# Kernel optimization log

Measured on AMD Instinct MI355X. Metric: run time of the kernel, lower is better.

The kernel has to match this reference:

```python
import jax, jax.numpy as jnp
import numpy as np

B, L = 4096, 4096

# 16 power-series exponents applied to each of the 4 physical params
PS_POWERS = jnp.array([-5.0, -4.0, -3.0, -2.0, -1.5, -1.0, -0.5, 0.0,
                       0.5, 2.0, 1.0/3.0, 3.0, 0.25, 4.0, 0.2, 5.0], dtype=jnp.float32)
# polynomial exponents of the ansatz y(eta)
POLY_POWERS = jnp.array([2.0, 5.0, 8.0, 11.0, 14.0], dtype=jnp.float32)


def setup_inputs() -> dict:
    key = jax.random.key(0)
    k1, k2, k3, k4, k5, k6 = jax.random.split(key, 6)
    # positive inputs: negative/fractional powers require x > 0
    physical_params = jax.random.uniform(k1, (B, 4), jnp.float32, minval=0.1, maxval=2.0)
    eta = jax.random.uniform(k2, (B, L), jnp.float32, minval=0.1, maxval=2.0)
    # MLP params: Linear(64, 32) and Linear(32, 5), torch layout [out, in]
    W1 = jax.random.normal(k3, (32, 64), jnp.float32) * (1.0 / np.sqrt(64.0))
    b1 = jax.random.normal(k4, (32,), jnp.float32) * 0.05
    W2 = jax.random.normal(k5, (5, 32), jnp.float32) * (1.0 / np.sqrt(32.0))
    b2 = jax.random.normal(k6, (5,), jnp.float32) * 0.05
    return {"physical_params": physical_params, "eta": eta,
            "W1": W1, "b1": b1, "W2": W2, "b2": b2}


def reference(physical_params, eta, W1, b1, W2, b2):
    # power-series transform: [B,4] -> [B,4,16] -> [B,64]
    t = (physical_params[:, :, None] ** PS_POWERS).reshape(physical_params.shape[0], -1)
    # global (scalar) normalization; torch .std() is unbiased (ddof=1)
    mean = t.mean()
    std = jnp.std(t, ddof=1)
    norm = (t - mean) / std
    # network = Sequential(ReLU, Linear(64,32), Linear(32,5)) -- ReLU first, no act between linears
    h = jnp.maximum(norm, 0.0) @ W1.T + b1            # [B, 32]
    coefficients = h @ W2.T + b2                       # [B, 5]
    # dy/deta[i,j] = sum_k c[i,k] * p_k * eta[i,j]^(p_k - 1)  (vectorizes the per-row loop)
    eta_pows = eta[:, :, None] ** (POLY_POWERS - 1.0)  # [B, L, 5]
    dy_deta = jnp.einsum('bk,bjk->bj', coefficients * POLY_POWERS, eta_pows)  # [B, L]
    return dy_deta
```

## Files before the change

### kernel.cpp

```cpp
#include <hip/hip_runtime.h>
#include <math.h>

static constexpr int B  = 4096;
static constexpr int L  = 4096;
static constexpr int NX = B * 4;
static constexpr int STATS_THREADS = 1024;

typedef float f4 __attribute__((ext_vector_type(4)));

__device__ __constant__ float c_ps_powers[16] = {
    -5.0f, -4.0f, -3.0f, -2.0f, -1.5f, -1.0f, -0.5f, 0.0f,
     0.5f,  2.0f,  0.33333334f, 3.0f, 0.25f, 4.0f, 0.2f, 5.0f};

__device__ __constant__ float c_poly[5] = {2.0f, 5.0f, 8.0f, 11.0f, 14.0f};

__device__ __forceinline__ float hw_log2(float x) { return __builtin_amdgcn_logf(x); }
__device__ __forceinline__ float hw_exp2(float x) { return __builtin_amdgcn_exp2f(x); }

__global__ __launch_bounds__(STATS_THREADS)
void k_stats(const float* __restrict__ pp, float* __restrict__ stats) {
    const int tid = threadIdx.x;
    const f4* pp4 = reinterpret_cast<const f4*>(pp);
    double s = 0.0, s2 = 0.0;
    #pragma unroll
    for (int k = 0; k < NX / 4 / STATS_THREADS; ++k) {
        const f4 xv = pp4[tid + k * STATS_THREADS];
        #pragma unroll
        for (int c = 0; c < 4; ++c) {
            const float lx = hw_log2(xv[c]);
            float sf = 0.0f, sf2 = 0.0f;
            #pragma unroll
            for (int p = 0; p < 16; ++p) {
                const float t = hw_exp2(c_ps_powers[p] * lx);
                sf  += t;
                sf2 = fmaf(t, t, sf2);
            }
            s  += (double)sf;
            s2 += (double)sf2;
        }
    }
    __shared__ double sh_s[STATS_THREADS];
    __shared__ double sh_s2[STATS_THREADS];
    sh_s[tid] = s; sh_s2[tid] = s2;
    __syncthreads();
    for (int off = STATS_THREADS >> 1; off > 0; off >>= 1) {
        if (tid < off) {
            sh_s[tid]  += sh_s[tid + off];
            sh_s2[tid] += sh_s2[tid + off];
        }
        __syncthreads();
    }
    if (tid == 0) {
        const double n    = (double)(B * 64);
        const double mean = sh_s[0] / n;
        const double var  = (sh_s2[0] - n * mean * mean) / (n - 1.0);
        stats[0] = (float)mean;
        stats[1] = (float)(1.0 / sqrt(var));
    }
}

__device__ __forceinline__ float poly_eval(float e, float c0, float c1,
                                           float c2, float c3, float c4) {
    const float e3 = e * e * e;
    float w   = e;
    float acc = c0 * w;
    w *= e3;
    acc = fmaf(c1, w, acc);
    w *= e3;
    acc = fmaf(c2, w, acc);
    w *= e3;
    acc = fmaf(c3, w, acc);
    w *= e3;
    acc = fmaf(c4, w, acc);
    return acc;
}

__device__ __forceinline__ f4 poly_eval4(f4 e, float c0, float c1,
                                         float c2, float c3, float c4) {
    f4 r;
    r.x = poly_eval(e.x, c0, c1, c2, c3, c4);
    r.y = poly_eval(e.y, c0, c1, c2, c3, c4);
    r.z = poly_eval(e.z, c0, c1, c2, c3, c4);
    r.w = poly_eval(e.w, c0, c1, c2, c3, c4);
    return r;
}

__global__ __launch_bounds__(256)
void k_main(const float* __restrict__ pp,  const float* __restrict__ eta,
            const float* __restrict__ W1,  const float* __restrict__ b1,
            const float* __restrict__ W2,  const float* __restrict__ b2,
            const float* __restrict__ stats, float* __restrict__ out) {
    const int row = blockIdx.x;
    const int tid = threadIdx.x;

    const f4* ep = reinterpret_cast<const f4*>(eta + (size_t)row * L);
    f4*       op = reinterpret_cast<f4*>(out + (size_t)row * L);
    const f4 e0 = ep[tid];
    const f4 e1 = ep[tid + 256];
    const f4 e2 = ep[tid + 512];
    const f4 e3 = ep[tid + 768];

    __shared__ float sh_r[64];
    __shared__ float sh_h[32];
    __shared__ float sh_c[8];

    if (tid < 64) {
        const float mean    = stats[0];
        const float inv_std = stats[1];
        const float x = pp[(row << 2) + (tid >> 4)];
        const float t = hw_exp2(c_ps_powers[tid & 15] * hw_log2(x));
        sh_r[tid] = fmaxf((t - mean) * inv_std, 0.0f);
    }
    __syncthreads();

    if (tid < 32) {
        float acc = b1[tid];
        const float* w = W1 + tid * 64;
        #pragma unroll
        for (int j = 0; j < 64; ++j) acc = fmaf(sh_r[j], w[j], acc);
        sh_h[tid] = acc;
    }
    __syncthreads();

    if (tid < 5) {
        float acc = b2[tid];
        const float* w = W2 + tid * 32;
        #pragma unroll
        for (int o = 0; o < 32; ++o) acc = fmaf(sh_h[o], w[o], acc);
        sh_c[tid] = acc * c_poly[tid];
    }
    __syncthreads();

    const float c0 = sh_c[0], c1 = sh_c[1], c2 = sh_c[2],
                c3 = sh_c[3], c4 = sh_c[4];

    op[tid]       = poly_eval4(e0, c0, c1, c2, c3, c4);
    op[tid + 256] = poly_eval4(e1, c0, c1, c2, c3, c4);
    op[tid + 512] = poly_eval4(e2, c0, c1, c2, c3, c4);
    op[tid + 768] = poly_eval4(e3, c0, c1, c2, c3, c4);
}

extern "C" void kernel_launch(void* const* d_in, const int* in_sizes, int n_in,
                              void* d_out, int out_size, void* d_ws, size_t ws_size,
                              hipStream_t stream) {
    const float* pp  = (const float*)d_in[0];
    const float* eta = (const float*)d_in[1];
    const float* W1  = (const float*)d_in[2];
    const float* b1  = (const float*)d_in[3];
    const float* W2  = (const float*)d_in[4];
    const float* b2  = (const float*)d_in[5];
    float* out = (float*)d_out;

    float* stats = (float*)d_ws;

    k_stats<<<1, STATS_THREADS, 0, stream>>>(pp, stats);
    k_main<<<B, 256, 0, stream>>>(pp, eta, W1, b1, W2, b2, stats, out);
}
```

Before: 41.27 us.

## Split global stats into 64-block partial sums reduced inside main kernel

Replaces the single-block statistics kernel with a 64-block kernel that writes per-block partial sums and sums of squares in double. Every main-kernel block then reduces the 64 partials with wave shuffles and computes mean and inverse std itself. This removes the serial single-workgroup stats pass that sat on the critical path before the main kernel. In exchange every one of the 4096 blocks repeats a small double-precision reduction and gains an extra barrier, and a leftover unused shuffle of a shared value stays in the code.

```diff
diff --git a/kernel.cpp b/kernel.cpp
--- a/kernel.cpp
+++ b/kernel.cpp
@@ -3,8 +3,7 @@
 
 static constexpr int B  = 4096;
 static constexpr int L  = 4096;
-static constexpr int NX = B * 4;
-static constexpr int STATS_THREADS = 1024;
+static constexpr int NPART = 64;
 
 typedef float f4 __attribute__((ext_vector_type(4)));
 
@@ -17,33 +16,24 @@
 __device__ __forceinline__ float hw_log2(float x) { return __builtin_amdgcn_logf(x); }
 __device__ __forceinline__ float hw_exp2(float x) { return __builtin_amdgcn_exp2f(x); }
 
-__global__ __launch_bounds__(STATS_THREADS)
-void k_stats(const float* __restrict__ pp, float* __restrict__ stats) {
+__global__ __launch_bounds__(256)
+void k_part(const float* __restrict__ pp, double* __restrict__ part) {
     const int tid = threadIdx.x;
-    const f4* pp4 = reinterpret_cast<const f4*>(pp);
-    double s = 0.0, s2 = 0.0;
+    const int g   = blockIdx.x * 256 + tid;
+    const float lx = hw_log2(pp[g]);
+    float sf = 0.0f, sf2 = 0.0f;
     #pragma unroll
-    for (int k = 0; k < NX / 4 / STATS_THREADS; ++k) {
-        const f4 xv = pp4[tid + k * STATS_THREADS];
-        #pragma unroll
-        for (int c = 0; c < 4; ++c) {
-            const float lx = hw_log2(xv[c]);
-            float sf = 0.0f, sf2 = 0.0f;
-            #pragma unroll
-            for (int p = 0; p < 16; ++p) {
-                const float t = hw_exp2(c_ps_powers[p] * lx);
-                sf  += t;
-                sf2 = fmaf(t, t, sf2);
-            }
-            s  += (double)sf;
-            s2 += (double)sf2;
-        }
+    for (int p = 0; p < 16; ++p) {
+        const float t = hw_exp2(c_ps_powers[p] * lx);
+        sf  += t;
+        sf2 = fmaf(t, t, sf2);
     }
-    __shared__ double sh_s[STATS_THREADS];
-    __shared__ double sh_s2[STATS_THREADS];
-    sh_s[tid] = s; sh_s2[tid] = s2;
+    __shared__ double sh_s[256];
+    __shared__ double sh_s2[256];
+    sh_s[tid]  = (double)sf;
+    sh_s2[tid] = (double)sf2;
     __syncthreads();
-    for (int off = STATS_THREADS >> 1; off > 0; off >>= 1) {
+    for (int off = 128; off > 0; off >>= 1) {
         if (tid < off) {
             sh_s[tid]  += sh_s[tid + off];
             sh_s2[tid] += sh_s2[tid + off];
@@ -51,11 +41,8 @@
         __syncthreads();
     }
     if (tid == 0) {
-        const double n    = (double)(B * 64);
-        const double mean = sh_s[0] / n;
-        const double var  = (sh_s2[0] - n * mean * mean) / (n - 1.0);
-        stats[0] = (float)mean;
-        stats[1] = (float)(1.0 / sqrt(var));
+        part[blockIdx.x]         = sh_s[0];
+        part[NPART + blockIdx.x] = sh_s2[0];
     }
 }
 
@@ -89,7 +76,7 @@
 void k_main(const float* __restrict__ pp,  const float* __restrict__ eta,
             const float* __restrict__ W1,  const float* __restrict__ b1,
             const float* __restrict__ W2,  const float* __restrict__ b2,
-            const float* __restrict__ stats, float* __restrict__ out) {
+            const double* __restrict__ part, float* __restrict__ out) {
     const int row = blockIdx.x;
     const int tid = threadIdx.x;
 
@@ -103,13 +90,33 @@
     __shared__ float sh_r[64];
     __shared__ float sh_h[32];
     __shared__ float sh_c[8];
+    __shared__ float sh_stat[2];
 
     if (tid < 64) {
-        const float mean    = stats[0];
-        const float inv_std = stats[1];
+        double s  = part[tid];
+        double s2 = part[NPART + tid];
+        #pragma unroll
+        for (int m = 32; m > 0; m >>= 1) {
+            s  += __shfl_xor(s,  m, 64);
+            s2 += __shfl_xor(s2, m, 64);
+        }
+        if (tid == 0) {
+            const double n    = 262144.0;
+            const double mean = s / n;
+            const double var  = (s2 - n * mean * mean) / (n - 1.0);
+            sh_stat[0] = (float)mean;
+            sh_stat[1] = (float)(1.0 / sqrt(var));
+        }
         const float x = pp[(row << 2) + (tid >> 4)];
         const float t = hw_exp2(c_ps_powers[tid & 15] * hw_log2(x));
-        sh_r[tid] = fmaxf((t - mean) * inv_std, 0.0f);
+        const float mean    = __shfl(sh_stat[0], 0, 64);
+        (void)mean;
+        sh_r[tid] = t;
+    }
+    __syncthreads();
+
+    if (tid < 64) {
+        sh_r[tid] = fmaxf((sh_r[tid] - sh_stat[0]) * sh_stat[1], 0.0f);
     }
     __syncthreads();
 
@@ -149,10 +156,9 @@
     const float* b1  = (const float*)d_in[3];
     const float* W2  = (const float*)d_in[4];
     const float* b2  = (const float*)d_in[5];
-    float* out = (float*)d_out;
+    float* out   = (float*)d_out;
+    double* part = (double*)d_ws;
 
-    float* stats = (float*)d_ws;
-
-    k_stats<<<1, STATS_THREADS, 0, stream>>>(pp, stats);
-    k_main<<<B, 256, 0, stream>>>(pp, eta, W1, b1, W2, b2, stats, out);
+    k_part<<<NPART, 256, 0, stream>>>(pp, part);
+    k_main<<<B, 256, 0, stream>>>(pp, eta, W1, b1, W2, b2, part, out);
 }
```

Result: faster. 33.78 us (-18.1%).
